# Kernel optimization log

Hardware: AMD Instinct MI355X
Metric: run time of the kernel (lower is better)

Reference implementation:

```python
import jax, jax.numpy as jnp
import numpy as np

GAMMA = 1.0 - 2.0 ** (-5)   # 0.96875, as in the module
NUM_GROUPS = 8
NUM_HEADS = 8
EPS = 1e-5


def setup_inputs() -> dict:
    key = jax.random.key(0)
    ks = jax.random.split(key, 8)
    M, S, Hd = 128, 512, 512  # num_segments, bonds per segment, hidden_size
    N = M * S
    return {
        "message": jax.random.normal(ks[0], (N, Hd), jnp.float32),
        "Wq": jax.random.normal(ks[1], (Hd, Hd), jnp.float32) / np.sqrt(Hd).astype(np.float32),
        "Wk": jax.random.normal(ks[2], (Hd, Hd), jnp.float32) / np.sqrt(Hd).astype(np.float32),
        "Wv": jax.random.normal(ks[3], (Hd, Hd), jnp.float32) / np.sqrt(Hd).astype(np.float32),
        "Wo": jax.random.normal(ks[4], (Hd, Hd), jnp.float32) / np.sqrt(Hd).astype(np.float32),
        "bo": jax.random.normal(ks[5], (Hd,), jnp.float32) * 0.01,
        "gn_w": jnp.ones((Hd,), jnp.float32),
        "gn_b": jnp.zeros((Hd,), jnp.float32),
        "num_segs": M,
        "seg_len": S,
    }


def _forward(message, Wq, Wk, Wv, Wo, bo, gn_w, gn_b, M, S):
    Hd = message.shape[1]
    H = NUM_HEADS
    d = Hd // H
    scale = jnp.float32(d ** (-0.5))
    gamma = jnp.float32(GAMMA)

    x = message.reshape(M, S, Hd)                       # equal contiguous segments
    q = (x @ Wq.T).reshape(M, S, H, d)
    k = (x @ Wk.T).reshape(M, S, H, d)
    v = (x @ Wv.T).reshape(M, S, H, d)

    # per-segment K^T V outer-product state contribution: [M, H, d, d]
    A = jnp.einsum('mshd,mshe->mhde', k, v)
    decay = gamma ** S  # gamma ** b_size for equal segments

    def step(r, a):
        # r = K_i^T V_i + gamma^{b_size} * r_prev  (state AFTER segment i, as in source)
        r_new = a + decay * r
        return r_new, r_new

    _, r_all = jax.lax.scan(step, jnp.zeros((H, d, d), x.dtype), A)  # [M, H, d, d]

    # intra-segment retention: (Q K^T) * scale @ V
    scores = jnp.einsum('mshd,mthd->mhst', q, k) * scale
    intra = jnp.einsum('mhst,mthd->mshd', scores, v)
    # cross/recurrent term: (Q @ r_i) * gamma^{i+1}  (note: NOT scaled by scale_factor)
    cross = jnp.einsum('mshd,mhde->mshe', q, r_all)
    g = (gamma ** jnp.arange(1, M + 1, dtype=jnp.float32))[:, None, None, None]
    h = jax.nn.relu(intra + cross * g)                  # activation; dropout p=0

    out = h.reshape(M, S, Hd) @ Wo.T + bo               # W_b_o
    res = x + out                                       # residual (dropout p=0)

    # GroupNorm(8, hidden): per segment (batch N=1), groups over hidden channels,
    # stats pooled over (hidden/8 group channels x S bonds)
    gsh = res.reshape(M, S, NUM_GROUPS, Hd // NUM_GROUPS)
    mean = gsh.mean(axis=(1, 3), keepdims=True)
    var = gsh.var(axis=(1, 3), keepdims=True)
    normed = ((gsh - mean) * jax.lax.rsqrt(var + EPS)).reshape(M, S, Hd)
    normed = normed * gn_w + gn_b

    flat = normed.reshape(M * S, Hd)
    # cached_zero_vector is prepended once before the first segment
    return jnp.concatenate([jnp.zeros((1, Hd), flat.dtype), flat], axis=0)


def reference(message, Wq, Wk, Wv, Wo, bo, gn_w, gn_b, num_segs, seg_len):
    return _forward(message, Wq, Wk, Wv, Wo, bo, gn_w, gn_b, num_segs, seg_len)
```

## Files before the change

### kernel.cpp

```cpp
#include <hip/hip_runtime.h>
#include <math.h>

#define M_SEG 128
#define S_SEG 512
#define HD 512
#define NHEAD 8
#define DHEAD 64
#define NROWS (M_SEG * S_SEG)
#define QKVLD 1536
#define GAMMA_F 0.96875f
#define SCALE_F 0.125f

typedef unsigned short u16;
typedef float f32x4 __attribute__((ext_vector_type(4)));
typedef __bf16 bf16x8 __attribute__((ext_vector_type(8)));
typedef unsigned short ushort8 __attribute__((ext_vector_type(8)));
typedef unsigned short ushort4v __attribute__((ext_vector_type(4)));

__device__ __forceinline__ u16 f2bf(float f) {
    union { float f; unsigned u; } x; x.f = f;
    unsigned r = x.u + 0x7FFFu + ((x.u >> 16) & 1u);
    return (u16)(r >> 16);
}
__device__ __forceinline__ float bf2f(u16 v) {
    union { unsigned u; float f; } x; x.u = ((unsigned)v) << 16;
    return x.f;
}

__device__ __forceinline__ void gload16(const u16* g, u16* l) {
    __builtin_amdgcn_global_load_lds(
        (const __attribute__((address_space(1))) void*)g,
        (__attribute__((address_space(3))) void*)l, 16, 0, 0);
}

__global__ __launch_bounds__(256) void convert_bf16(const float* __restrict__ in,
                                                    u16* __restrict__ outp, int n8)
{
    int idx = blockIdx.x * 256 + threadIdx.x;
    if (idx >= n8) return;
    const float4 a = *reinterpret_cast<const float4*>(&in[(size_t)idx * 8]);
    const float4 b = *reinterpret_cast<const float4*>(&in[(size_t)idx * 8 + 4]);
    ushort8 o;
    o[0] = f2bf(a.x); o[1] = f2bf(a.y); o[2] = f2bf(a.z); o[3] = f2bf(a.w);
    o[4] = f2bf(b.x); o[5] = f2bf(b.y); o[6] = f2bf(b.z); o[7] = f2bf(b.w);
    *reinterpret_cast<ushort8*>(&outp[(size_t)idx * 8]) = o;
}

__global__ __launch_bounds__(256) void convert_weights(const float* __restrict__ w0,
                                                       const float* __restrict__ w1,
                                                       const float* __restrict__ w2,
                                                       const float* __restrict__ w3,
                                                       u16* __restrict__ outp)
{
    const int which = blockIdx.y;
    const float* src = which == 0 ? w0 : which == 1 ? w1 : which == 2 ? w2 : w3;
    u16* dst = outp + (size_t)which * 262144;
    int idx = blockIdx.x * 256 + threadIdx.x;
    const float4 a = *reinterpret_cast<const float4*>(&src[(size_t)idx * 8]);
    const float4 b = *reinterpret_cast<const float4*>(&src[(size_t)idx * 8 + 4]);
    ushort8 o;
    o[0] = f2bf(a.x); o[1] = f2bf(a.y); o[2] = f2bf(a.z); o[3] = f2bf(a.w);
    o[4] = f2bf(b.x); o[5] = f2bf(b.y); o[6] = f2bf(b.z); o[7] = f2bf(b.w);
    *reinterpret_cast<ushort8*>(&dst[(size_t)idx * 8]) = o;
}

template<int EPI>
__global__ __launch_bounds__(512, 1) void gemm8x(const u16* __restrict__ A, int lda,
                                                 const u16* __restrict__ B,
                                                 u16* __restrict__ Cv, int ldc, int ntile,
                                                 const u16* __restrict__ Xb,
                                                 const float* __restrict__ bias)
{
    __shared__ __align__(16) u16 sm[65536];
    const int t    = threadIdx.x;
    const int lane = t & 63;
    const int w    = t >> 6;
    const int wm   = w >> 2;
    const int wn   = w & 3;

    const int nwg  = gridDim.x;
    const int cpx  = nwg >> 3;
    const int bid  = blockIdx.x;
    const int sbid = (bid & 7) * cpx + (bid >> 3);
    const int mt = sbid / ntile, nt = sbid % ntile;
    const int rowBase = mt * 256, colBase = nt * 256;

    const int frow = lane & 15;
    const int fkc  = lane >> 4;
    const int orow = (lane >> 4) * 4;

    const int r0  = t >> 3;
    const int ksl = (t & 7) ^ (r0 & 7);

    f32x4 acc[8][4];
#pragma unroll
    for (int i = 0; i < 8; ++i)
#pragma unroll
        for (int j = 0; j < 4; ++j)
            acc[i][j] = (f32x4){0.f, 0.f, 0.f, 0.f};

#define STG(Mp, ld_, base_, kt, L, b, reg)                                    \
    do {                                                                      \
        u16* d_ = &sm[(b) * 32768 + (reg) * 16384 + (L) * 8192];              \
        const u16* s_ = &Mp[(size_t)(base_ + (L) * 128 + r0) * (ld_)          \
                            + (kt) * 64 + ksl * 8];                           \
        gload16(s_, &d_[t * 8]);                                              \
        gload16(s_ + (size_t)64 * (ld_), &d_[4096 + t * 8]);                  \
    } while (0)
#define STG_A(kt, L, b) STG(A, lda, rowBase, kt, L, b, 0)
#define STG_B(kt, L, b) STG(B, HD, colBase, kt, L, b, 1)

#define FRD_A(dst, b, mm0)                                                    \
    do {                                                                      \
        const u16* h_ = &sm[(b) * 32768 + wm * 8192];                         \
        _Pragma("unroll")                                                     \
        for (int q_ = 0; q_ < 4; ++q_)                                        \
            _Pragma("unroll")                                                 \
            for (int ks_ = 0; ks_ < 2; ++ks_) {                               \
                const int row_ = ((mm0) + q_) * 16 + frow;                    \
                const int sl_ = (ks_ * 4 + fkc) ^ (row_ & 7);                 \
                dst[q_][ks_] = *reinterpret_cast<const bf16x8*>(              \
                    &h_[row_ * 64 + sl_ * 8]);                                \
            }                                                                 \
    } while (0)
#define FRD_B(dst, b, nn0)                                                    \
    do {                                                                      \
        const u16* h_ = &sm[(b) * 32768 + 16384 + (wn >> 1) * 8192];          \
        _Pragma("unroll")                                                     \
        for (int q_ = 0; q_ < 2; ++q_)                                        \
            _Pragma("unroll")                                                 \
            for (int ks_ = 0; ks_ < 2; ++ks_) {                               \
                const int row_ = (wn & 1) * 64 + ((nn0) + q_) * 16 + frow;    \
                const int sl_ = (ks_ * 4 + fkc) ^ (row_ & 7);                 \
                dst[q_][ks_] = *reinterpret_cast<const bf16x8*>(              \
                    &h_[row_ * 64 + sl_ * 8]);                                \
            }                                                                 \
    } while (0)
#define MFQ(m0, n0, aA, bA)                                                   \
    do {                                                                      \
        __builtin_amdgcn_s_setprio(1);                                        \
        _Pragma("unroll")                                                     \
        for (int mm_ = 0; mm_ < 4; ++mm_)                                     \
            _Pragma("unroll")                                                 \
            for (int nn_ = 0; nn_ < 2; ++nn_)                                 \
                _Pragma("unroll")                                             \
                for (int ks_ = 0; ks_ < 2; ++ks_)                             \
                    acc[(m0) + mm_][(n0) + nn_] =                             \
                        __builtin_amdgcn_mfma_f32_16x16x32_bf16(              \
                            aA[mm_][ks_], bA[nn_][ks_],                       \
                            acc[(m0) + mm_][(n0) + nn_], 0, 0, 0);            \
        __builtin_amdgcn_s_setprio(0);                                        \
    } while (0)
#define BARW()                                                                \
    do {                                                                      \
        __builtin_amdgcn_s_barrier();                                         \
        asm volatile("s_waitcnt lgkmcnt(0)" ::: "memory");                    \
        __builtin_amdgcn_sched_barrier(0);                                    \
    } while (0)
#define BAR() __builtin_amdgcn_s_barrier()

    STG_A(0, 0, 0); STG_A(0, 1, 0); STG_B(0, 0, 0); STG_B(0, 1, 0);
    STG_A(1, 0, 1);
    asm volatile("s_waitcnt vmcnt(2)" ::: "memory");
    BAR();

    bf16x8 aL[4][2], aH[4][2], bLo[2][2], bHi[2][2];

#pragma unroll 1
    for (int j = 0; j < 4; ++j) {
        const int te = 2 * j, to = 2 * j + 1;
        FRD_A(aL, 0, 0); FRD_B(bLo, 0, 0);
        STG_A(to, 1, 1);
        BARW(); MFQ(0, 0, aL, bLo); BAR();
        FRD_B(bHi, 0, 2);
        STG_B(to, 0, 1);
        BARW(); MFQ(0, 2, aL, bHi); BAR();
        FRD_A(aH, 0, 4);
        STG_B(to, 1, 1);
        BARW(); MFQ(4, 0, aH, bLo); BAR();
        if (j < 3) {
            STG_A(te + 2, 0, 0);
            asm volatile("s_waitcnt vmcnt(2)" ::: "memory");
        } else {
            asm volatile("s_waitcnt vmcnt(0)" ::: "memory");
        }
        BAR(); MFQ(4, 2, aH, bHi); BAR();
        FRD_A(aL, 1, 0); FRD_B(bLo, 1, 0);
        if (j < 3) STG_A(te + 2, 1, 0);
        BARW(); MFQ(0, 0, aL, bLo); BAR();
        FRD_B(bHi, 1, 2);
        if (j < 3) STG_B(te + 2, 0, 0);
        BARW(); MFQ(0, 2, aL, bHi); BAR();
        FRD_A(aH, 1, 4);
        if (j < 3) STG_B(te + 2, 1, 0);
        BARW(); MFQ(4, 0, aH, bLo); BAR();
        if (j < 3) {
            STG_A(to + 2, 0, 1);
            asm volatile("s_waitcnt vmcnt(2)" ::: "memory");
        }
        BAR(); MFQ(4, 2, aH, bHi); BAR();
    }
#undef STG
#undef STG_A
#undef STG_B
#undef FRD_A
#undef FRD_B
#undef MFQ
#undef BARW
#undef BAR

    if (EPI == 0) {
        u16* ldsC = sm;
#pragma unroll
        for (int hp = 0; hp < 2; ++hp) {
            __syncthreads();
            if (wm == hp) {
#pragma unroll
                for (int mm = 0; mm < 8; ++mm)
#pragma unroll
                    for (int nn = 0; nn < 4; ++nn) {
                        const int row0 = mm * 16 + orow;
                        const int col  = wn * 64 + nn * 16 + frow;
#pragma unroll
                        for (int r = 0; r < 4; ++r)
                            ldsC[(row0 + r) * 256 + col] = f2bf(acc[mm][nn][r]);
                    }
            }
            __syncthreads();
#pragma unroll
            for (int p = 0; p < 8; ++p) {
                const int lin = p * 512 + t;
                const int row = lin >> 5, c8 = lin & 31;
                *reinterpret_cast<ushort8*>(
                    &Cv[(size_t)(rowBase + hp * 128 + row) * ldc + colBase + c8 * 8]) =
                    *reinterpret_cast<const ushort8*>(&ldsC[row * 256 + c8 * 8]);
            }
        }
    } else {
        float* ldsF = (float*)sm;
#pragma unroll
        for (int q = 0; q < 4; ++q) {
            __syncthreads();
            if (wm == (q >> 1)) {
#pragma unroll
                for (int mm = 0; mm < 4; ++mm) {
                    const int macc = (q & 1) * 4 + mm;
#pragma unroll
                    for (int nn = 0; nn < 4; ++nn) {
                        const int row0 = mm * 16 + orow;
                        const int col  = wn * 64 + nn * 16 + frow;
#pragma unroll
                        for (int r = 0; r < 4; ++r)
                            ldsF[(row0 + r) * 256 + col] = acc[macc][nn][r];
                    }
                }
            }
            __syncthreads();
#pragma unroll
            for (int p = 0; p < 8; ++p) {
                const int lin = p * 512 + t;
                const int row = lin >> 6, c4 = lin & 63;
                const int grow = rowBase + q * 64 + row;
                float4 a = *reinterpret_cast<const float4*>(&ldsF[row * 256 + c4 * 4]);
                ushort4v x4 = *reinterpret_cast<const ushort4v*>(
                    &Xb[(size_t)grow * HD + colBase + c4 * 4]);
                float4 b = *reinterpret_cast<const float4*>(&bias[colBase + c4 * 4]);
                ushort4v o;
                o[0] = f2bf(a.x + bf2f(x4[0]) + b.x);
                o[1] = f2bf(a.y + bf2f(x4[1]) + b.y);
                o[2] = f2bf(a.z + bf2f(x4[2]) + b.z);
                o[3] = f2bf(a.w + bf2f(x4[3]) + b.w);
                *reinterpret_cast<ushort4v*>(
                    &Cv[(size_t)grow * ldc + colBase + c4 * 4]) = o;
            }
        }
    }
}

__global__ __launch_bounds__(256) void kv_outer_mfma(const u16* __restrict__ qkv,
                                                     float* __restrict__ Abuf)
{
    __shared__ __align__(16) u16 kT[2048];
    __shared__ __align__(16) u16 vT[2048];
    const int t    = threadIdx.x;
    const int lane = t & 63;
    const int w    = t >> 6;
    const int hh   = blockIdx.x;
    const int m    = blockIdx.y;
    const int sl   = t & 31;
    const int dg   = (t >> 5) * 8;
    const int frow = lane & 15, fkc = lane >> 4, orow = (lane >> 4) * 4;
    const size_t gbase = (size_t)(m * S_SEG) * QKVLD + 512 + hh * DHEAD + dg;

    f32x4 acc[4];
#pragma unroll
    for (int i = 0; i < 4; ++i) acc[i] = (f32x4){0.f, 0.f, 0.f, 0.f};

    ushort8 ka, va, kb, vb;

#define LOADC(c, K8, V8)                                                      \
    do {                                                                      \
        size_t g_ = gbase + (size_t)((c) * 32 + sl) * QKVLD;                  \
        K8 = *reinterpret_cast<const ushort8*>(&qkv[g_]);                     \
        V8 = *reinterpret_cast<const ushort8*>(&qkv[g_ + 512]);               \
    } while (0)
#define WRTC(K8, V8)                                                          \
    do {                                                                      \
        _Pragma("unroll")                                                     \
        for (int j = 0; j < 8; ++j) {                                         \
            const int d_ = dg + j;                                            \
            const int a_ = d_ * 32 + ((((sl >> 3) ^ ((d_ >> 1) & 3))) << 3) + (sl & 7); \
            kT[a_] = K8[j];                                                   \
            vT[a_] = V8[j];                                                   \
        }                                                                     \
    } while (0)
#define CMPC()                                                                \
    do {                                                                      \
        bf16x8 kf[4], vf;                                                     \
        _Pragma("unroll")                                                     \
        for (int mf = 0; mf < 4; ++mf) {                                      \
            const int d_ = mf * 16 + frow;                                    \
            kf[mf] = *reinterpret_cast<const bf16x8*>(                        \
                &kT[d_ * 32 + ((fkc ^ ((d_ >> 1) & 3)) << 3)]);               \
        }                                                                     \
        const int e_ = w * 16 + frow;                                         \
        vf = *reinterpret_cast<const bf16x8*>(                                \
            &vT[e_ * 32 + ((fkc ^ ((e_ >> 1) & 3)) << 3)]);                   \
        _Pragma("unroll")                                                     \
        for (int mf = 0; mf < 4; ++mf)                                        \
            acc[mf] = __builtin_amdgcn_mfma_f32_16x16x32_bf16(kf[mf], vf, acc[mf], 0, 0, 0); \
    } while (0)

    LOADC(0, ka, va);
#pragma unroll 1
    for (int cc = 0; cc < 16; cc += 2) {
        WRTC(ka, va);
        LOADC(cc + 1, kb, vb);
        asm volatile("s_waitcnt lgkmcnt(0)" ::: "memory");
        __builtin_amdgcn_s_barrier();
        __builtin_amdgcn_sched_barrier(0);
        CMPC();
        __builtin_amdgcn_s_barrier();

        WRTC(kb, vb);
        if (cc + 2 < 16) LOADC(cc + 2, ka, va);
        asm volatile("s_waitcnt lgkmcnt(0)" ::: "memory");
        __builtin_amdgcn_s_barrier();
        __builtin_amdgcn_sched_barrier(0);
        CMPC();
        __builtin_amdgcn_s_barrier();
    }
#undef LOADC
#undef WRTC
#undef CMPC

    const size_t hb = (size_t)(m * NHEAD + hh) * DHEAD * DHEAD;
#pragma unroll
    for (int mf = 0; mf < 4; ++mf)
#pragma unroll
        for (int r = 0; r < 4; ++r)
            Abuf[hb + (size_t)(mf * 16 + orow + r) * DHEAD + w * 16 + frow] = acc[mf][r];
}

__global__ __launch_bounds__(256) void scan_kernel(const float* __restrict__ Abuf,
                                                   float* __restrict__ Bc)
{
    const int tid = blockIdx.x * 256 + threadIdx.x;
    const float decay = powf(GAMMA_F, (float)S_SEG);
    float r = 0.0f;
    float g = 1.0f;
    for (int m = 0; m < M_SEG; ++m) {
        float a = Abuf[(size_t)m * 32768 + tid];
        r = fmaf(decay, r, a);
        g *= GAMMA_F;
        Bc[(size_t)m * 32768 + tid] = fmaf(g, r, SCALE_F * a);
    }
}

__global__ __launch_bounds__(256) void h_mfma(u16* __restrict__ qkv,
                                              const float* __restrict__ Bc)
{
    __shared__ __align__(16) u16 BT[64 * 72];
    const int t    = threadIdx.x;
    const int lane = t & 63;
    const int w    = t >> 6;
    const int m    = blockIdx.y;
    const int sBase = blockIdx.x * 256 + w * 64;
    const int frow = lane & 15;
    const int fkc  = lane >> 4;

    for (int hh = 0; hh < NHEAD; ++hh) {
#pragma unroll
        for (int i = 0; i < 4; ++i) {
            int idx = t + i * 256;
            int d = idx >> 4, e4 = idx & 15;
            float4 v = *reinterpret_cast<const float4*>(
                &Bc[((size_t)(m * NHEAD + hh) * DHEAD + d) * DHEAD + e4 * 4]);
            BT[(e4 * 4 + 0) * 72 + d] = f2bf(v.x);
            BT[(e4 * 4 + 1) * 72 + d] = f2bf(v.y);
            BT[(e4 * 4 + 2) * 72 + d] = f2bf(v.z);
            BT[(e4 * 4 + 3) * 72 + d] = f2bf(v.w);
        }
        __syncthreads();

        f32x4 acc[4][4];
#pragma unroll
        for (int i = 0; i < 4; ++i)
#pragma unroll
            for (int j = 0; j < 4; ++j)
                acc[i][j] = (f32x4){0.f, 0.f, 0.f, 0.f};

#pragma unroll
        for (int ks = 0; ks < 2; ++ks) {
            bf16x8 af[4], bfr[4];
#pragma unroll
            for (int mm = 0; mm < 4; ++mm) {
                const int grow = m * S_SEG + sBase + mm * 16 + frow;
                af[mm] = *reinterpret_cast<const bf16x8*>(
                    &qkv[(size_t)grow * QKVLD + hh * DHEAD + ks * 32 + fkc * 8]);
                const int e = mm * 16 + frow;
                bfr[mm] = *reinterpret_cast<const bf16x8*>(&BT[e * 72 + ks * 32 + fkc * 8]);
            }
#pragma unroll
            for (int mm = 0; mm < 4; ++mm)
#pragma unroll
                for (int nn = 0; nn < 4; ++nn)
                    acc[mm][nn] = __builtin_amdgcn_mfma_f32_16x16x32_bf16(af[mm], bfr[nn], acc[mm][nn], 0, 0, 0);
        }

        const int orow = (lane >> 4) * 4;
#pragma unroll
        for (int mm = 0; mm < 4; ++mm)
#pragma unroll
            for (int nn = 0; nn < 4; ++nn) {
                const int col  = hh * DHEAD + nn * 16 + frow;
                const int row0 = m * S_SEG + sBase + mm * 16 + orow;
#pragma unroll
                for (int r = 0; r < 4; ++r)
                    qkv[(size_t)(row0 + r) * QKVLD + col] = f2bf(fmaxf(acc[mm][nn][r], 0.f));
            }
        __syncthreads();
    }
}

__global__ __launch_bounds__(256) void groupnorm_bf16(const u16* __restrict__ res,
                                                      float* __restrict__ out,
                                                      const float* __restrict__ gn_w,
                                                      const float* __restrict__ gn_b)
{
    const int g = blockIdx.x;
    const int m = blockIdx.y;
    const int t = threadIdx.x;
    const u16* base = res + (size_t)(m * S_SEG) * QKVLD + g * DHEAD;

    float sum = 0.0f, sq = 0.0f;
    for (int idx = t; idx < 4096; idx += 256) {
        int s = idx >> 3, c8 = idx & 7;
        ushort8 v = *reinterpret_cast<const ushort8*>(&base[(size_t)s * QKVLD + c8 * 8]);
#pragma unroll
        for (int j = 0; j < 8; ++j) {
            float f = bf2f(v[j]);
            sum += f; sq += f * f;
        }
    }
    __shared__ float rs[256], rq[256];
    rs[t] = sum; rq[t] = sq;
    __syncthreads();
    for (int off = 128; off > 0; off >>= 1) {
        if (t < off) { rs[t] += rs[t + off]; rq[t] += rq[t + off]; }
        __syncthreads();
    }
    __shared__ float smean, sinv;
    if (t == 0) {
        float mean = rs[0] * (1.0f / 32768.0f);
        float var  = rq[0] * (1.0f / 32768.0f) - mean * mean;
        smean = mean;
        sinv  = rsqrtf(var + 1e-5f);
    }
    __syncthreads();
    const float mean = smean, inv = sinv;

    for (int idx = t; idx < 4096; idx += 256) {
        int s = idx >> 3, c8 = idx & 7;
        ushort8 v = *reinterpret_cast<const ushort8*>(&base[(size_t)s * QKVLD + c8 * 8]);
        float o[8];
#pragma unroll
        for (int j = 0; j < 8; ++j) {
            float wj = gn_w[g * DHEAD + c8 * 8 + j];
            float bj = gn_b[g * DHEAD + c8 * 8 + j];
            o[j] = (bf2f(v[j]) - mean) * inv * wj + bj;
        }
        float* dst = &out[(size_t)(1 + m * S_SEG + s) * HD + g * DHEAD + c8 * 8];
        *reinterpret_cast<float4*>(dst)     = make_float4(o[0], o[1], o[2], o[3]);
        *reinterpret_cast<float4*>(dst + 4) = make_float4(o[4], o[5], o[6], o[7]);
    }
}

__global__ void zero_row(float* __restrict__ out)
{
    int i = blockIdx.x * 256 + threadIdx.x;
    if (i < HD) out[i] = 0.0f;
}

extern "C" void kernel_launch(void* const* d_in, const int* in_sizes, int n_in,
                              void* d_out, int out_size, void* d_ws, size_t ws_size,
                              hipStream_t stream)
{
    const float* msg = (const float*)d_in[0];
    const float* Wq  = (const float*)d_in[1];
    const float* Wk  = (const float*)d_in[2];
    const float* Wv  = (const float*)d_in[3];
    const float* Wo  = (const float*)d_in[4];
    const float* bo  = (const float*)d_in[5];
    const float* gnw = (const float*)d_in[6];
    const float* gnb = (const float*)d_in[7];
    float* out = (float*)d_out;

    u16*   msgb = (u16*)out;
    float* Abuf = out + 16777216;
    float* Bc   = out + 16777216 + 4194304;

    u16* Wb   = (u16*)d_ws;
    u16* qkv  = Wb + 4 * 262144;
    u16* resB = qkv + 512;

    convert_weights<<<dim3(128, 4), 256, 0, stream>>>(Wq, Wk, Wv, Wo, Wb);
    convert_bf16<<<16384, 256, 0, stream>>>(msg, msgb, 4194304);

    gemm8x<0><<<1536, 512, 0, stream>>>(msgb, HD, Wb, qkv, QKVLD, 6, nullptr, nullptr);

    kv_outer_mfma<<<dim3(NHEAD, M_SEG), 256, 0, stream>>>(qkv, Abuf);
    scan_kernel<<<128, 256, 0, stream>>>(Abuf, Bc);
    h_mfma<<<dim3(2, M_SEG), 256, 0, stream>>>(qkv, Bc);

    gemm8x<1><<<512, 512, 0, stream>>>(qkv, QKVLD, Wb + 3 * 262144, resB, QKVLD, 2, msgb, bo);

    zero_row<<<2, 256, 0, stream>>>(out);
    groupnorm_bf16<<<dim3(8, M_SEG), 256, 0, stream>>>(resB, out, gnw, gnb);
}
```

Measured before the change: 367.2 us.

## Replace 256x256 GEMM with 128x128 multi-block GEMM, add split-bf16 state matmul

Replaces the 512-thread 256x256-tile hand-scheduled GEMM with a simpler 256-thread 128x128-tile double-buffered kernel that allows four blocks per CU. The intent is better occupancy and latency hiding in place of the intricate per-subtile barrier schedule. The output GEMM's residual now reads the fp32 message directly instead of the bf16 copy, which adds global traffic but improves accuracy. h_mfma splits the state matrix into hi and lo bf16 parts, doubling its MFMAs for precision. Compiler fences are also added after barriers in another kernel.

```diff
diff --git a/kernel.cpp b/kernel.cpp
--- a/kernel.cpp
+++ b/kernel.cpp
@@ -25,6 +25,11 @@
 __device__ __forceinline__ float bf2f(u16 v) {
     union { unsigned u; float f; } x; x.u = ((unsigned)v) << 16;
     return x.f;
+}
+
+__device__ __forceinline__ void fence_all() {
+    asm volatile("" ::: "memory");
+    __builtin_amdgcn_sched_barrier(0);
 }
 
 __device__ __forceinline__ void gload16(const u16* g, u16* l) {
@@ -65,211 +70,144 @@
 }
 
 template<int EPI>
-__global__ __launch_bounds__(512, 1) void gemm8x(const u16* __restrict__ A, int lda,
+__global__ __launch_bounds__(256, 4) void gemm4b(const u16* __restrict__ A, int lda,
                                                  const u16* __restrict__ B,
                                                  u16* __restrict__ Cv, int ldc, int ntile,
-                                                 const u16* __restrict__ Xb,
+                                                 const float* __restrict__ Xf,
                                                  const float* __restrict__ bias)
 {
-    __shared__ __align__(16) u16 sm[65536];
+    __shared__ __align__(16) u16 sm[2][8192];
     const int t    = threadIdx.x;
     const int lane = t & 63;
     const int w    = t >> 6;
-    const int wm   = w >> 2;
-    const int wn   = w & 3;
+    const int wm   = w >> 1;
+    const int wn   = w & 1;
 
     const int nwg  = gridDim.x;
     const int cpx  = nwg >> 3;
     const int bid  = blockIdx.x;
     const int sbid = (bid & 7) * cpx + (bid >> 3);
     const int mt = sbid / ntile, nt = sbid % ntile;
-    const int rowBase = mt * 256, colBase = nt * 256;
-
-    const int frow = lane & 15;
-    const int fkc  = lane >> 4;
-    const int orow = (lane >> 4) * 4;
-
-    const int r0  = t >> 3;
-    const int ksl = (t & 7) ^ (r0 & 7);
-
-    f32x4 acc[8][4];
-#pragma unroll
-    for (int i = 0; i < 8; ++i)
+    const int rowBase = mt * 128, colBase = nt * 128;
+
+    const int frow = lane & 15, fkc = lane >> 4, orow = (lane >> 4) * 4;
+
+    const int sr0 = t >> 2;
+    const int ksl = (t & 3) ^ ((sr0 >> 1) & 3);
+
+    const size_t gA0 = (size_t)(rowBase + sr0)      * lda + ksl * 8;
+    const size_t gA1 = (size_t)(rowBase + sr0 + 64) * lda + ksl * 8;
+    const size_t gB0 = (size_t)(colBase + sr0)      * HD  + ksl * 8;
+    const size_t gB1 = (size_t)(colBase + sr0 + 64) * HD  + ksl * 8;
+
+    f32x4 acc[4][4];
+#pragma unroll
+    for (int i = 0; i < 4; ++i)
 #pragma unroll
         for (int j = 0; j < 4; ++j)
             acc[i][j] = (f32x4){0.f, 0.f, 0.f, 0.f};
 
-#define STG(Mp, ld_, base_, kt, L, b, reg)                                    \
+#define STAGE(kt, buf)                                                        \
     do {                                                                      \
-        u16* d_ = &sm[(b) * 32768 + (reg) * 16384 + (L) * 8192];              \
-        const u16* s_ = &Mp[(size_t)(base_ + (L) * 128 + r0) * (ld_)          \
-                            + (kt) * 64 + ksl * 8];                           \
-        gload16(s_, &d_[t * 8]);                                              \
-        gload16(s_ + (size_t)64 * (ld_), &d_[4096 + t * 8]);                  \
+        gload16(&A[gA0 + (kt) * 32], &sm[buf][t * 8]);                        \
+        gload16(&A[gA1 + (kt) * 32], &sm[buf][2048 + t * 8]);                 \
+        gload16(&B[gB0 + (kt) * 32], &sm[buf][4096 + t * 8]);                 \
+        gload16(&B[gB1 + (kt) * 32], &sm[buf][6144 + t * 8]);                 \
     } while (0)
-#define STG_A(kt, L, b) STG(A, lda, rowBase, kt, L, b, 0)
-#define STG_B(kt, L, b) STG(B, HD, colBase, kt, L, b, 1)
-
-#define FRD_A(dst, b, mm0)                                                    \
-    do {                                                                      \
-        const u16* h_ = &sm[(b) * 32768 + wm * 8192];                         \
-        _Pragma("unroll")                                                     \
-        for (int q_ = 0; q_ < 4; ++q_)                                        \
-            _Pragma("unroll")                                                 \
-            for (int ks_ = 0; ks_ < 2; ++ks_) {                               \
-                const int row_ = ((mm0) + q_) * 16 + frow;                    \
-                const int sl_ = (ks_ * 4 + fkc) ^ (row_ & 7);                 \
-                dst[q_][ks_] = *reinterpret_cast<const bf16x8*>(              \
-                    &h_[row_ * 64 + sl_ * 8]);                                \
-            }                                                                 \
-    } while (0)
-#define FRD_B(dst, b, nn0)                                                    \
-    do {                                                                      \
-        const u16* h_ = &sm[(b) * 32768 + 16384 + (wn >> 1) * 8192];          \
-        _Pragma("unroll")                                                     \
-        for (int q_ = 0; q_ < 2; ++q_)                                        \
-            _Pragma("unroll")                                                 \
-            for (int ks_ = 0; ks_ < 2; ++ks_) {                               \
-                const int row_ = (wn & 1) * 64 + ((nn0) + q_) * 16 + frow;    \
-                const int sl_ = (ks_ * 4 + fkc) ^ (row_ & 7);                 \
-                dst[q_][ks_] = *reinterpret_cast<const bf16x8*>(              \
-                    &h_[row_ * 64 + sl_ * 8]);                                \
-            }                                                                 \
-    } while (0)
-#define MFQ(m0, n0, aA, bA)                                                   \
-    do {                                                                      \
-        __builtin_amdgcn_s_setprio(1);                                        \
-        _Pragma("unroll")                                                     \
-        for (int mm_ = 0; mm_ < 4; ++mm_)                                     \
-            _Pragma("unroll")                                                 \
-            for (int nn_ = 0; nn_ < 2; ++nn_)                                 \
-                _Pragma("unroll")                                             \
-                for (int ks_ = 0; ks_ < 2; ++ks_)                             \
-                    acc[(m0) + mm_][(n0) + nn_] =                             \
-                        __builtin_amdgcn_mfma_f32_16x16x32_bf16(              \
-                            aA[mm_][ks_], bA[nn_][ks_],                       \
-                            acc[(m0) + mm_][(n0) + nn_], 0, 0, 0);            \
-        __builtin_amdgcn_s_setprio(0);                                        \
-    } while (0)
-#define BARW()                                                                \
-    do {                                                                      \
-        __builtin_amdgcn_s_barrier();                                         \
-        asm volatile("s_waitcnt lgkmcnt(0)" ::: "memory");                    \
-        __builtin_amdgcn_sched_barrier(0);                                    \
-    } while (0)
-#define BAR() __builtin_amdgcn_s_barrier()
-
-    STG_A(0, 0, 0); STG_A(0, 1, 0); STG_B(0, 0, 0); STG_B(0, 1, 0);
-    STG_A(1, 0, 1);
-    asm volatile("s_waitcnt vmcnt(2)" ::: "memory");
-    BAR();
-
-    bf16x8 aL[4][2], aH[4][2], bLo[2][2], bHi[2][2];
+
+    STAGE(0, 0);
+    STAGE(1, 1);
 
 #pragma unroll 1
-    for (int j = 0; j < 4; ++j) {
-        const int te = 2 * j, to = 2 * j + 1;
-        FRD_A(aL, 0, 0); FRD_B(bLo, 0, 0);
-        STG_A(to, 1, 1);
-        BARW(); MFQ(0, 0, aL, bLo); BAR();
-        FRD_B(bHi, 0, 2);
-        STG_B(to, 0, 1);
-        BARW(); MFQ(0, 2, aL, bHi); BAR();
-        FRD_A(aH, 0, 4);
-        STG_B(to, 1, 1);
-        BARW(); MFQ(4, 0, aH, bLo); BAR();
-        if (j < 3) {
-            STG_A(te + 2, 0, 0);
-            asm volatile("s_waitcnt vmcnt(2)" ::: "memory");
-        } else {
-            asm volatile("s_waitcnt vmcnt(0)" ::: "memory");
-        }
-        BAR(); MFQ(4, 2, aH, bHi); BAR();
-        FRD_A(aL, 1, 0); FRD_B(bLo, 1, 0);
-        if (j < 3) STG_A(te + 2, 1, 0);
-        BARW(); MFQ(0, 0, aL, bLo); BAR();
-        FRD_B(bHi, 1, 2);
-        if (j < 3) STG_B(te + 2, 0, 0);
-        BARW(); MFQ(0, 2, aL, bHi); BAR();
-        FRD_A(aH, 1, 4);
-        if (j < 3) STG_B(te + 2, 1, 0);
-        BARW(); MFQ(4, 0, aH, bLo); BAR();
-        if (j < 3) {
-            STG_A(to + 2, 0, 1);
-            asm volatile("s_waitcnt vmcnt(2)" ::: "memory");
-        }
-        BAR(); MFQ(4, 2, aH, bHi); BAR();
-    }
-#undef STG
-#undef STG_A
-#undef STG_B
-#undef FRD_A
-#undef FRD_B
-#undef MFQ
-#undef BARW
-#undef BAR
+    for (int kt = 0; kt < 16; ++kt) {
+        const int buf = kt & 1;
+        if (kt < 15) asm volatile("s_waitcnt vmcnt(4)" ::: "memory");
+        else         asm volatile("s_waitcnt vmcnt(0)" ::: "memory");
+        __builtin_amdgcn_s_barrier();
+        fence_all();
+
+        const u16* Ab = sm[buf];
+        const u16* Bb = sm[buf] + 4096;
+        bf16x8 af[4], bfv[4];
+#pragma unroll
+        for (int mm = 0; mm < 4; ++mm) {
+            const int r = wm * 64 + mm * 16 + frow;
+            af[mm] = *reinterpret_cast<const bf16x8*>(
+                &Ab[r * 32 + ((fkc ^ ((r >> 1) & 3)) << 3)]);
+        }
+#pragma unroll
+        for (int nn = 0; nn < 4; ++nn) {
+            const int r = wn * 64 + nn * 16 + frow;
+            bfv[nn] = *reinterpret_cast<const bf16x8*>(
+                &Bb[r * 32 + ((fkc ^ ((r >> 1) & 3)) << 3)]);
+        }
+        __builtin_amdgcn_s_setprio(1);
+#pragma unroll
+        for (int mm = 0; mm < 4; ++mm)
+#pragma unroll
+            for (int nn = 0; nn < 4; ++nn)
+                acc[mm][nn] = __builtin_amdgcn_mfma_f32_16x16x32_bf16(af[mm], bfv[nn], acc[mm][nn], 0, 0, 0);
+        __builtin_amdgcn_s_setprio(0);
+
+        __builtin_amdgcn_s_barrier();
+        fence_all();
+        if (kt < 14) STAGE(kt + 2, buf);
+    }
+#undef STAGE
 
     if (EPI == 0) {
-        u16* ldsC = sm;
-#pragma unroll
-        for (int hp = 0; hp < 2; ++hp) {
+        u16* ldsC = (u16*)sm;
+#pragma unroll
+        for (int mm = 0; mm < 4; ++mm)
+#pragma unroll
+            for (int nn = 0; nn < 4; ++nn) {
+                const int row0 = wm * 64 + mm * 16 + orow;
+                const int col  = wn * 64 + nn * 16 + frow;
+#pragma unroll
+                for (int r = 0; r < 4; ++r)
+                    ldsC[(row0 + r) * 128 + col] = f2bf(acc[mm][nn][r]);
+            }
+        __syncthreads();
+#pragma unroll
+        for (int p = 0; p < 8; ++p) {
+            const int lin = p * 256 + t;
+            const int row = lin >> 4, c8 = lin & 15;
+            *reinterpret_cast<ushort8*>(
+                &Cv[(size_t)(rowBase + row) * ldc + colBase + c8 * 8]) =
+                *reinterpret_cast<const ushort8*>(&ldsC[row * 128 + c8 * 8]);
+        }
+    } else {
+        float* ldsF = (float*)sm;
+#pragma unroll
+        for (int half = 0; half < 2; ++half) {
             __syncthreads();
-            if (wm == hp) {
-#pragma unroll
-                for (int mm = 0; mm < 8; ++mm)
+            if (wm == half) {
+#pragma unroll
+                for (int mm = 0; mm < 4; ++mm)
 #pragma unroll
                     for (int nn = 0; nn < 4; ++nn) {
                         const int row0 = mm * 16 + orow;
                         const int col  = wn * 64 + nn * 16 + frow;
 #pragma unroll
                         for (int r = 0; r < 4; ++r)
-                            ldsC[(row0 + r) * 256 + col] = f2bf(acc[mm][nn][r]);
+                            ldsF[(row0 + r) * 128 + col] = acc[mm][nn][r];
                     }
             }
             __syncthreads();
 #pragma unroll
             for (int p = 0; p < 8; ++p) {
-                const int lin = p * 512 + t;
-                const int row = lin >> 5, c8 = lin & 31;
-                *reinterpret_cast<ushort8*>(
-                    &Cv[(size_t)(rowBase + hp * 128 + row) * ldc + colBase + c8 * 8]) =
-                    *reinterpret_cast<const ushort8*>(&ldsC[row * 256 + c8 * 8]);
-            }
-        }
-    } else {
-        float* ldsF = (float*)sm;
-#pragma unroll
-        for (int q = 0; q < 4; ++q) {
-            __syncthreads();
-            if (wm == (q >> 1)) {
-#pragma unroll
-                for (int mm = 0; mm < 4; ++mm) {
-                    const int macc = (q & 1) * 4 + mm;
-#pragma unroll
-                    for (int nn = 0; nn < 4; ++nn) {
-                        const int row0 = mm * 16 + orow;
-                        const int col  = wn * 64 + nn * 16 + frow;
-#pragma unroll
-                        for (int r = 0; r < 4; ++r)
-                            ldsF[(row0 + r) * 256 + col] = acc[macc][nn][r];
-                    }
-                }
-            }
-            __syncthreads();
-#pragma unroll
-            for (int p = 0; p < 8; ++p) {
-                const int lin = p * 512 + t;
-                const int row = lin >> 6, c4 = lin & 63;
-                const int grow = rowBase + q * 64 + row;
-                float4 a = *reinterpret_cast<const float4*>(&ldsF[row * 256 + c4 * 4]);
-                ushort4v x4 = *reinterpret_cast<const ushort4v*>(
-                    &Xb[(size_t)grow * HD + colBase + c4 * 4]);
+                const int lin = p * 256 + t;
+                const int row = lin >> 5, c4 = lin & 31;
+                const int grow = rowBase + half * 64 + row;
+                float4 a = *reinterpret_cast<const float4*>(&ldsF[row * 128 + c4 * 4]);
+                float4 x = *reinterpret_cast<const float4*>(
+                    &Xf[(size_t)grow * HD + colBase + c4 * 4]);
                 float4 b = *reinterpret_cast<const float4*>(&bias[colBase + c4 * 4]);
                 ushort4v o;
-                o[0] = f2bf(a.x + bf2f(x4[0]) + b.x);
-                o[1] = f2bf(a.y + bf2f(x4[1]) + b.y);
-                o[2] = f2bf(a.z + bf2f(x4[2]) + b.z);
-                o[3] = f2bf(a.w + bf2f(x4[3]) + b.w);
+                o[0] = f2bf(a.x + x.x + b.x);
+                o[1] = f2bf(a.y + x.y + b.y);
+                o[2] = f2bf(a.z + x.z + b.z);
+                o[3] = f2bf(a.w + x.w + b.w);
                 *reinterpret_cast<ushort4v*>(
                     &Cv[(size_t)grow * ldc + colBase + c4 * 4]) = o;
             }
@@ -341,6 +279,7 @@
         __builtin_amdgcn_sched_barrier(0);
         CMPC();
         __builtin_amdgcn_s_barrier();
+        fence_all();
 
         WRTC(kb, vb);
         if (cc + 2 < 16) LOADC(cc + 2, ka, va);
@@ -349,6 +288,7 @@
         __builtin_amdgcn_sched_barrier(0);
         CMPC();
         __builtin_amdgcn_s_barrier();
+        fence_all();
     }
 #undef LOADC
 #undef WRTC
@@ -380,7 +320,8 @@
 __global__ __launch_bounds__(256) void h_mfma(u16* __restrict__ qkv,
                                               const float* __restrict__ Bc)
 {
-    __shared__ __align__(16) u16 BT[64 * 72];
+    __shared__ __align__(16) u16 BTh[64 * 72];
+    __shared__ __align__(16) u16 BTl[64 * 72];
     const int t    = threadIdx.x;
     const int lane = t & 63;
     const int w    = t >> 6;
@@ -396,10 +337,13 @@
             int d = idx >> 4, e4 = idx & 15;
             float4 v = *reinterpret_cast<const float4*>(
                 &Bc[((size_t)(m * NHEAD + hh) * DHEAD + d) * DHEAD + e4 * 4]);
-            BT[(e4 * 4 + 0) * 72 + d] = f2bf(v.x);
-            BT[(e4 * 4 + 1) * 72 + d] = f2bf(v.y);
-            BT[(e4 * 4 + 2) * 72 + d] = f2bf(v.z);
-            BT[(e4 * 4 + 3) * 72 + d] = f2bf(v.w);
+            float vv[4] = {v.x, v.y, v.z, v.w};
+#pragma unroll
+            for (int j = 0; j < 4; ++j) {
+                u16 hi = f2bf(vv[j]);
+                BTh[(e4 * 4 + j) * 72 + d] = hi;
+                BTl[(e4 * 4 + j) * 72 + d] = f2bf(vv[j] - bf2f(hi));
+            }
         }
         __syncthreads();
 
@@ -412,20 +356,23 @@
 
 #pragma unroll
         for (int ks = 0; ks < 2; ++ks) {
-            bf16x8 af[4], bfr[4];
+            bf16x8 af[4], bh[4], bl[4];
 #pragma unroll
             for (int mm = 0; mm < 4; ++mm) {
                 const int grow = m * S_SEG + sBase + mm * 16 + frow;
                 af[mm] = *reinterpret_cast<const bf16x8*>(
                     &qkv[(size_t)grow * QKVLD + hh * DHEAD + ks * 32 + fkc * 8]);
                 const int e = mm * 16 + frow;
-                bfr[mm] = *reinterpret_cast<const bf16x8*>(&BT[e * 72 + ks * 32 + fkc * 8]);
+                bh[mm] = *reinterpret_cast<const bf16x8*>(&BTh[e * 72 + ks * 32 + fkc * 8]);
+                bl[mm] = *reinterpret_cast<const bf16x8*>(&BTl[e * 72 + ks * 32 + fkc * 8]);
             }
 #pragma unroll
             for (int mm = 0; mm < 4; ++mm)
 #pragma unroll
-                for (int nn = 0; nn < 4; ++nn)
-                    acc[mm][nn] = __builtin_amdgcn_mfma_f32_16x16x32_bf16(af[mm], bfr[nn], acc[mm][nn], 0, 0, 0);
+                for (int nn = 0; nn < 4; ++nn) {
+                    acc[mm][nn] = __builtin_amdgcn_mfma_f32_16x16x32_bf16(af[mm], bl[nn], acc[mm][nn], 0, 0, 0);
+                    acc[mm][nn] = __builtin_amdgcn_mfma_f32_16x16x32_bf16(af[mm], bh[nn], acc[mm][nn], 0, 0, 0);
+                }
         }
 
         const int orow = (lane >> 4) * 4;
@@ -527,13 +474,13 @@
     convert_weights<<<dim3(128, 4), 256, 0, stream>>>(Wq, Wk, Wv, Wo, Wb);
     convert_bf16<<<16384, 256, 0, stream>>>(msg, msgb, 4194304);
 
-    gemm8x<0><<<1536, 512, 0, stream>>>(msgb, HD, Wb, qkv, QKVLD, 6, nullptr, nullptr);
+    gemm4b<0><<<6144, 256, 0, stream>>>(msgb, HD, Wb, qkv, QKVLD, 12, nullptr, nullptr);
 
     kv_outer_mfma<<<dim3(NHEAD, M_SEG), 256, 0, stream>>>(qkv, Abuf);
     scan_kernel<<<128, 256, 0, stream>>>(Abuf, Bc);
     h_mfma<<<dim3(2, M_SEG), 256, 0, stream>>>(qkv, Bc);
 
-    gemm8x<1><<<512, 512, 0, stream>>>(qkv, QKVLD, Wb + 3 * 262144, resB, QKVLD, 2, msgb, bo);
+    gemm4b<1><<<2048, 256, 0, stream>>>(qkv, QKVLD, Wb + 3 * 262144, resB, QKVLD, 4, msg, bo);
 
     zero_row<<<2, 256, 0, stream>>>(out);
     groupnorm_bf16<<<dim3(8, M_SEG), 256, 0, stream>>>(resB, out, gnw, gnb);
```

Measured after the change: 376.1 us. 1.02x slower.
